# Optimization experiments

Measured on AMD Instinct MI355X. Metric: run time of the kernel, lower is better.

Reference implementation:

```python
import jax, jax.numpy as jnp
import numpy as np

N = 100000      # nodes
E = 1600000     # edges
F = 128         # num_node_features
C = 64          # graph_hidden_channels
NH = 256        # nhid
NOUT = 128      # nout
L = 4           # n_layers (hidden GCN layers)
G = 512         # number of graphs in batch


def setup_inputs() -> dict:
    key = jax.random.key(0)
    ks = jax.random.split(key, 10)
    x = jax.random.normal(ks[0], (N, F), jnp.float32)
    edge_index = jax.random.randint(ks[1], (2, E), 0, N, dtype=jnp.int64)
    batch = jnp.sort(jax.random.randint(ks[2], (N,), 0, G, dtype=jnp.int64))

    def w(k, shape, fan_in):
        return jax.random.normal(k, shape, jnp.float32) / np.float32(np.sqrt(fan_in))

    W0 = w(ks[3], (F, C), F)
    b0 = jnp.zeros((C,), jnp.float32)
    Wh = w(ks[4], (L, C, C), C)      # stacked hidden GCN weights
    bh = jnp.zeros((L, C), jnp.float32)
    W1 = w(ks[5], (C, NH), C)
    b1 = jnp.zeros((NH,), jnp.float32)
    W2 = w(ks[6], (NH, NOUT), NH)
    b2 = jnp.zeros((NOUT,), jnp.float32)
    return dict(x=x, edge_index=edge_index, batch=batch,
                W0=W0, b0=b0, Wh=Wh, bh=bh, W1=W1, b1=b1, W2=W2, b2=b2)


def _gcn_conv(h_in, W, b, src, dst, dinv):
    # PyG GCNConv: out_i = sum_{j->i} dinv_j * dinv_i * (x_j W) + dinv_i^2 * (x_i W) + b
    h = h_in @ W                                   # [N, C]
    coef = (dinv[src] * dinv[dst])[:, None]        # [E, 1]
    agg = jax.ops.segment_sum(h[src] * coef, dst, num_segments=N)
    agg = agg + h * (dinv * dinv)[:, None]         # self-loop term
    return agg + b


def reference(x, edge_index, batch, W0, b0, Wh, bh, W1, b1, W2, b2):
    src, dst = edge_index[0], edge_index[1]
    # degree with self loops (edge weight 1)
    deg = jax.ops.segment_sum(jnp.ones((E,), x.dtype), dst, num_segments=N) + 1.0
    dinv = jax.lax.rsqrt(deg)                      # [N]

    h = jax.nn.relu(_gcn_conv(x, W0, b0, src, dst, dinv))
    for i in range(L):
        h = jax.nn.relu(_gcn_conv(h, Wh[i], bh[i], src, dst, dinv))

    # global mean pool over graphs
    counts = jax.ops.segment_sum(jnp.ones((N,), x.dtype), batch, num_segments=G)
    pooled = jax.ops.segment_sum(h, batch, num_segments=G) / jnp.maximum(counts, 1.0)[:, None]

    out = jax.nn.relu(pooled @ W1 + b1)
    out = out @ W2 + b2
    return out
```

## Files before the change

kernel.cpp:

```cpp
#include <hip/hip_runtime.h>
#include <hip/hip_fp16.h>
#include <stddef.h>

static constexpr int Nn    = 100000;
static constexpr int Ee    = 1600000;
static constexpr int Ff    = 128;
static constexpr int Cc    = 64;
static constexpr int NHh   = 256;
static constexpr int NOUTt = 128;
static constexpr int Ll    = 4;
static constexpr int Gg    = 512;

static constexpr int SCAN_BLK = 1024;
static constexpr int NBLK_SCAN = (Nn + SCAN_BLK - 1) / SCAN_BLK;

static constexpr int NSUB   = (Nn + 511) / 512;
static constexpr int SUBCAP = 10240;

__global__ __launch_bounds__(256) void bin_kernel(const int* __restrict__ src,
                                                  const int* __restrict__ dst,
                                                  int* __restrict__ sb,
                                                  int* __restrict__ scnt, int E) {
    __shared__ int lcnt[NSUB], lbase[NSUB];
    const int tid = threadIdx.x;
    for (int i = tid; i < NSUB; i += 256) lcnt[i] = 0;
    __syncthreads();
    const int base = blockIdx.x * 2048;
    int pk[8], ps[8], lr[8];
    #pragma unroll
    for (int i = 0; i < 8; ++i) {
        int e = base + i * 256 + tid;
        if (e < E) {
            int d = dst[e], s = src[e];
            int sub = d >> 9;
            ps[i] = sub;
            pk[i] = s | ((d & 511) << 17);
            lr[i] = atomicAdd(&lcnt[sub], 1);
        } else ps[i] = -1;
    }
    __syncthreads();
    for (int i = tid; i < NSUB; i += 256) lbase[i] = atomicAdd(&scnt[i], lcnt[i]);
    __syncthreads();
    #pragma unroll
    for (int i = 0; i < 8; ++i) {
        if (ps[i] >= 0) {
            int pos = lbase[ps[i]] + lr[i];
            if (pos < SUBCAP) sb[(size_t)ps[i] * SUBCAP + pos] = pk[i];
        }
    }
}

__global__ __launch_bounds__(512) void cnt3_kernel(const int* __restrict__ sb,
                                                   const int* __restrict__ scnt,
                                                   int* __restrict__ cnt) {
    __shared__ int lcnt[512];
    const int sub = blockIdx.x, tid = threadIdx.x;
    lcnt[tid] = 0;
    __syncthreads();
    const int n = scnt[sub];
    const int* bp = sb + (size_t)sub * SUBCAP;
    for (int i = tid; i < n; i += 512) atomicAdd(&lcnt[(bp[i] >> 17) & 511], 1);
    __syncthreads();
    int node = sub * 512 + tid;
    if (node < Nn) cnt[node] = lcnt[tid];
}

__global__ void dinv_kernel(const int* __restrict__ cnt, float* __restrict__ dinv, int n) {
    int i = blockIdx.x * blockDim.x + threadIdx.x;
    if (i < n) dinv[i] = rsqrtf((float)cnt[i] + 1.0f);
}

__global__ __launch_bounds__(SCAN_BLK) void scan1_kernel(const int* __restrict__ cnt,
                                                         int* __restrict__ row_off,
                                                         int* __restrict__ bsum, int n) {
    __shared__ int sd[SCAN_BLK];
    int tid = threadIdx.x;
    int gid = blockIdx.x * SCAN_BLK + tid;
    int v = (gid < n) ? cnt[gid] : 0;
    sd[tid] = v;
    __syncthreads();
    #pragma unroll
    for (int off = 1; off < SCAN_BLK; off <<= 1) {
        int t = (tid >= off) ? sd[tid - off] : 0;
        __syncthreads();
        sd[tid] += t;
        __syncthreads();
    }
    if (gid < n) row_off[gid + 1] = sd[tid];
    if (tid == SCAN_BLK - 1) bsum[blockIdx.x] = sd[tid];
}

__global__ __launch_bounds__(128) void scan2_kernel(const int* __restrict__ bsum,
                                                    int* __restrict__ boff, int nb) {
    __shared__ int sd[128];
    int tid = threadIdx.x;
    sd[tid] = (tid < nb) ? bsum[tid] : 0;
    __syncthreads();
    #pragma unroll
    for (int off = 1; off < 128; off <<= 1) {
        int t = (tid >= off) ? sd[tid - off] : 0;
        __syncthreads();
        sd[tid] += t;
        __syncthreads();
    }
    if (tid < nb) boff[tid] = (tid == 0) ? 0 : sd[tid - 1];
}

__global__ void scan3_kernel(int* __restrict__ row_off, const int* __restrict__ boff, int n) {
    int gid = blockIdx.x * blockDim.x + threadIdx.x;
    if (gid < n) row_off[gid + 1] += boff[gid >> 10];
    if (gid == 0) row_off[0] = 0;
}

__global__ __launch_bounds__(512) void fill3_kernel(const int* __restrict__ sb,
                                                    const int* __restrict__ scnt,
                                                    const int* __restrict__ roff,
                                                    int* __restrict__ csr) {
    __shared__ int lcnt[512], lofs[512];
    __shared__ int gbase;
    const int sub = blockIdx.x, tid = threadIdx.x;
    lcnt[tid] = 0;
    if (tid == 0) gbase = roff[sub * 512];
    __syncthreads();
    const int n = scnt[sub];
    const int* bp = sb + (size_t)sub * SUBCAP;
    for (int i = tid; i < n; i += 512) atomicAdd(&lcnt[(bp[i] >> 17) & 511], 1);
    __syncthreads();
    int v = lcnt[tid];
    lofs[tid] = v;
    __syncthreads();
    #pragma unroll
    for (int off = 1; off < 512; off <<= 1) {
        int t = (tid >= off) ? lofs[tid - off] : 0;
        __syncthreads();
        lofs[tid] += t;
        __syncthreads();
    }
    int excl = lofs[tid] - v;
    __syncthreads();
    lcnt[tid] = excl;
    __syncthreads();
    for (int i = tid; i < n; i += 512) {
        int e = bp[i];
        int pos = atomicAdd(&lcnt[(e >> 17) & 511], 1);
        csr[gbase + pos] = e & 0x1FFFF;
    }
}

__device__ inline void add_h8(float acc[8], float4 raw) {
    const __half2* hp = reinterpret_cast<const __half2*>(&raw);
    #pragma unroll
    for (int j = 0; j < 4; ++j) {
        float2 f = __half22float2(hp[j]);
        acc[2 * j]     += f.x;
        acc[2 * j + 1] += f.y;
    }
}

__device__ inline void cvt_h8(float4 raw, float v[8]) {
    const __half2* hp = reinterpret_cast<const __half2*>(&raw);
    #pragma unroll
    for (int j = 0; j < 4; ++j) {
        float2 f = __half22float2(hp[j]);
        v[2 * j] = f.x; v[2 * j + 1] = f.y;
    }
}

__global__ __launch_bounds__(256) void gemm_xw_f32(const float* __restrict__ X,
                                                   const float* __restrict__ W,
                                                   const float* __restrict__ dinv,
                                                   __half* __restrict__ Y, int n) {
    __shared__ float hs[64][68];
    __shared__ float ws[64][64];
    const int tid = threadIdx.x;
    const int tx  = tid & 15;
    const int ty  = tid >> 4;
    const int rowbase = blockIdx.x * 64;

    float acc[4][4] = {};

    for (int k0 = 0; k0 < Ff; k0 += 64) {
        #pragma unroll
        for (int i = 0; i < 4; ++i) {
            int r = ty + i * 16;
            int gr = rowbase + r;
            float4 v = make_float4(0.f, 0.f, 0.f, 0.f);
            if (gr < n) v = *(const float4*)(X + (size_t)gr * Ff + k0 + tx * 4);
            *(float4*)&hs[r][tx * 4] = v;
        }
        #pragma unroll
        for (int i = 0; i < 4; ++i) {
            int k = ty + i * 16;
            *(float4*)&ws[k][tx * 4] = *(const float4*)(W + (size_t)(k0 + k) * 64 + tx * 4);
        }
        __syncthreads();

        #pragma unroll 4
        for (int k = 0; k < 64; ++k) {
            float4 w = *(const float4*)&ws[k][tx * 4];
            float h0 = hs[ty * 4 + 0][k];
            float h1 = hs[ty * 4 + 1][k];
            float h2 = hs[ty * 4 + 2][k];
            float h3 = hs[ty * 4 + 3][k];
            acc[0][0] += h0 * w.x; acc[0][1] += h0 * w.y; acc[0][2] += h0 * w.z; acc[0][3] += h0 * w.w;
            acc[1][0] += h1 * w.x; acc[1][1] += h1 * w.y; acc[1][2] += h1 * w.z; acc[1][3] += h1 * w.w;
            acc[2][0] += h2 * w.x; acc[2][1] += h2 * w.y; acc[2][2] += h2 * w.z; acc[2][3] += h2 * w.w;
            acc[3][0] += h3 * w.x; acc[3][1] += h3 * w.y; acc[3][2] += h3 * w.z; acc[3][3] += h3 * w.w;
        }
        __syncthreads();
    }

    #pragma unroll
    for (int i = 0; i < 4; ++i) {
        int gr = rowbase + ty * 4 + i;
        if (gr < n) {
            float di = dinv[gr];
            __half2 p0 = __floats2half2_rn(acc[i][0] * di, acc[i][1] * di);
            __half2 p1 = __floats2half2_rn(acc[i][2] * di, acc[i][3] * di);
            float2 st;
            *reinterpret_cast<__half2*>(&st.x) = p0;
            *reinterpret_cast<__half2*>(&st.y) = p1;
            *reinterpret_cast<float2*>(Y + (size_t)gr * 64 + tx * 4) = st;
        }
    }
}

__global__ __launch_bounds__(256) void gemm_xw_f16(const __half* __restrict__ X,
                                                   const float* __restrict__ W,
                                                   const float* __restrict__ dinv,
                                                   __half* __restrict__ Y, int n) {
    __shared__ float hs[64][68];
    __shared__ float ws[64][64];
    const int tid = threadIdx.x;
    const int tx  = tid & 15;
    const int ty  = tid >> 4;
    const int rowbase = blockIdx.x * 64;

    float acc[4][4] = {};

    #pragma unroll
    for (int i = 0; i < 4; ++i) {
        int r = ty + i * 16;
        int gr = rowbase + r;
        float4 v = make_float4(0.f, 0.f, 0.f, 0.f);
        if (gr < n) {
            float2 raw = *(const float2*)(X + (size_t)gr * 64 + tx * 4);
            __half2 a = *reinterpret_cast<__half2*>(&raw.x);
            __half2 b = *reinterpret_cast<__half2*>(&raw.y);
            float2 fa = __half22float2(a), fb = __half22float2(b);
            v = make_float4(fa.x, fa.y, fb.x, fb.y);
        }
        *(float4*)&hs[r][tx * 4] = v;
    }
    #pragma unroll
    for (int i = 0; i < 4; ++i) {
        int k = ty + i * 16;
        *(float4*)&ws[k][tx * 4] = *(const float4*)(W + (size_t)k * 64 + tx * 4);
    }
    __syncthreads();

    #pragma unroll 4
    for (int k = 0; k < 64; ++k) {
        float4 w = *(const float4*)&ws[k][tx * 4];
        float h0 = hs[ty * 4 + 0][k];
        float h1 = hs[ty * 4 + 1][k];
        float h2 = hs[ty * 4 + 2][k];
        float h3 = hs[ty * 4 + 3][k];
        acc[0][0] += h0 * w.x; acc[0][1] += h0 * w.y; acc[0][2] += h0 * w.z; acc[0][3] += h0 * w.w;
        acc[1][0] += h1 * w.x; acc[1][1] += h1 * w.y; acc[1][2] += h1 * w.z; acc[1][3] += h1 * w.w;
        acc[2][0] += h2 * w.x; acc[2][1] += h2 * w.y; acc[2][2] += h2 * w.z; acc[2][3] += h2 * w.w;
        acc[3][0] += h3 * w.x; acc[3][1] += h3 * w.y; acc[3][2] += h3 * w.z; acc[3][3] += h3 * w.w;
    }

    #pragma unroll
    for (int i = 0; i < 4; ++i) {
        int gr = rowbase + ty * 4 + i;
        if (gr < n) {
            float di = dinv[gr];
            __half2 p0 = __floats2half2_rn(acc[i][0] * di, acc[i][1] * di);
            __half2 p1 = __floats2half2_rn(acc[i][2] * di, acc[i][3] * di);
            float2 st;
            *reinterpret_cast<__half2*>(&st.x) = p0;
            *reinterpret_cast<__half2*>(&st.y) = p1;
            *reinterpret_cast<float2*>(Y + (size_t)gr * 64 + tx * 4) = st;
        }
    }
}

__global__ __launch_bounds__(256) void gather_agg(const int* __restrict__ row_off,
                                                  const int* __restrict__ csr_src,
                                                  const float* __restrict__ dinv,
                                                  const __half* __restrict__ t,
                                                  const float* __restrict__ b,
                                                  __half* __restrict__ out, int n) {
    const int lane = threadIdx.x & 63;
    const int node = (blockIdx.x * blockDim.x + threadIdx.x) >> 6;
    if (node >= n) return;
    const int sub = lane >> 3;
    const int c8  = lane & 7;

    const int base = row_off[node];
    const int end  = row_off[node + 1];

    float acc[8] = {};

    for (int k0 = base; k0 < end; k0 += 64) {
        int myidx = (k0 + lane < end) ? csr_src[k0 + lane] : 0;
        int nk = min(64, end - k0);
        int k = 0;
        for (; k + 16 <= nk; k += 16) {
            int s0 = __shfl(myidx, k + sub);
            int s1 = __shfl(myidx, k + 8 + sub);
            float4 r0 = *(const float4*)(t + (size_t)s0 * 64 + c8 * 8);
            float4 r1 = *(const float4*)(t + (size_t)s1 * 64 + c8 * 8);
            add_h8(acc, r0);
            add_h8(acc, r1);
        }
        for (; k < nk; k += 8) {
            int kk = k + sub;
            int s = __shfl(myidx, kk);
            if (kk < nk) {
                float4 r = *(const float4*)(t + (size_t)s * 64 + c8 * 8);
                add_h8(acc, r);
            }
        }
    }

    #pragma unroll
    for (int off = 8; off < 64; off <<= 1) {
        #pragma unroll
        for (int j = 0; j < 8; ++j) acc[j] += __shfl_xor(acc[j], off);
    }

    if (sub == 0) {
        float di = dinv[node];
        float selfv[8];
        cvt_h8(*(const float4*)(t + (size_t)node * 64 + c8 * 8), selfv);
        float4 b0 = *(const float4*)(b + c8 * 8);
        float4 b1 = *(const float4*)(b + c8 * 8 + 4);
        float bb[8] = {b0.x, b0.y, b0.z, b0.w, b1.x, b1.y, b1.z, b1.w};
        __half2 o[4];
        #pragma unroll
        for (int j = 0; j < 4; ++j) {
            float v0 = fmaxf(di * (acc[2 * j]     + selfv[2 * j])     + bb[2 * j],     0.f);
            float v1 = fmaxf(di * (acc[2 * j + 1] + selfv[2 * j + 1]) + bb[2 * j + 1], 0.f);
            o[j] = __floats2half2_rn(v0, v1);
        }
        *(float4*)(out + (size_t)node * 64 + c8 * 8) = *reinterpret_cast<float4*>(o);
    }
}

__global__ void gbounds_kernel(const int* __restrict__ batch, int* __restrict__ gstart, int n) {
    int i = blockIdx.x * blockDim.x + threadIdx.x;
    if (i >= n) return;
    int bi = batch[i];
    int bp = (i == 0) ? -1 : batch[i - 1];
    for (int g = bp + 1; g <= bi; ++g) gstart[g] = i;
    if (i == n - 1) {
        for (int g = bi + 1; g <= Gg; ++g) gstart[g] = n;
    }
}

__global__ __launch_bounds__(256) void pool_graph(const __half* __restrict__ h,
                                                  const int* __restrict__ gstart,
                                                  float* __restrict__ pooled) {
    __shared__ float sd[4][64];
    const int g    = blockIdx.x;
    const int lane = threadIdx.x & 63;
    const int wv   = threadIdx.x >> 6;
    const int s = gstart[g], e = gstart[g + 1];
    float acc = 0.f;
    for (int i = s + wv; i < e; i += 4) acc += __half2float(h[(size_t)i * 64 + lane]);
    sd[wv][lane] = acc;
    __syncthreads();
    if (wv == 0) {
        float sum = sd[0][lane] + sd[1][lane] + sd[2][lane] + sd[3][lane];
        float c = (float)(e - s);
        pooled[(size_t)g * 64 + lane] = sum / fmaxf(c, 1.f);
    }
}

__global__ void mlp1_kernel(const float* __restrict__ P, const float* __restrict__ W1,
                            const float* __restrict__ b1, float* __restrict__ H) {
    int gid = blockIdx.x * blockDim.x + threadIdx.x;
    if (gid >= Gg * NHh) return;
    int j = gid & (NHh - 1), g = gid >> 8;
    const float* p = P + (size_t)g * Cc;
    float s = b1[j];
    #pragma unroll 8
    for (int k = 0; k < Cc; ++k) s += p[k] * W1[(size_t)k * NHh + j];
    H[gid] = fmaxf(s, 0.f);
}

__global__ void mlp2_kernel(const float* __restrict__ H, const float* __restrict__ W2,
                            const float* __restrict__ b2, float* __restrict__ O) {
    int gid = blockIdx.x * blockDim.x + threadIdx.x;
    if (gid >= Gg * NOUTt) return;
    int j = gid & (NOUTt - 1), g = gid >> 7;
    const float* h = H + (size_t)g * NHh;
    float s = b2[j];
    #pragma unroll 8
    for (int k = 0; k < NHh; ++k) s += h[k] * W2[(size_t)k * NOUTt + j];
    O[gid] = s;
}

extern "C" void kernel_launch(void* const* d_in, const int* in_sizes, int n_in,
                              void* d_out, int out_size, void* d_ws, size_t ws_size,
                              hipStream_t stream) {
    const float* x     = (const float*)d_in[0];
    const int*   ei    = (const int*)  d_in[1];
    const int*   batch = (const int*)  d_in[2];
    const float* W0    = (const float*)d_in[3];
    const float* b0    = (const float*)d_in[4];
    const float* Wh    = (const float*)d_in[5];
    const float* bh    = (const float*)d_in[6];
    const float* W1    = (const float*)d_in[7];
    const float* b1    = (const float*)d_in[8];
    const float* W2    = (const float*)d_in[9];
    const float* b2    = (const float*)d_in[10];

    const int* src = ei;
    const int* dst = ei + Ee;

    char* ws = (char*)d_ws;
    constexpr size_t OFF_DINV  = 0;
    constexpr size_t OFF_CNT   = 400384;
    constexpr size_t OFF_ROFF  = OFF_CNT + 400384;
    constexpr size_t OFF_BSUM  = OFF_ROFF + 400384;
    constexpr size_t OFF_BOFF  = OFF_BSUM + 1024;
    constexpr size_t OFF_SCNT  = OFF_BOFF + 1024;
    constexpr size_t OFF_CSR   = OFF_SCNT + 1024;
    constexpr size_t OFF_T     = OFF_CSR + 6400256;
    constexpr size_t OFF_A     = OFF_T + 12800256;
    constexpr size_t OFF_POOL  = OFF_A + 12800256;
    constexpr size_t OFF_GST   = OFF_POOL + (size_t)Gg * Cc * 4;
    constexpr size_t OFF_HID   = OFF_GST + 4096;
    const size_t OFF_SB = OFF_T;

    float*  dinv   = (float*) (ws + OFF_DINV);
    int*    cnt    = (int*)   (ws + OFF_CNT);
    int*    roff   = (int*)   (ws + OFF_ROFF);
    int*    bsum   = (int*)   (ws + OFF_BSUM);
    int*    boff   = (int*)   (ws + OFF_BOFF);
    int*    scnt   = (int*)   (ws + OFF_SCNT);
    int*    csrs   = (int*)   (ws + OFF_CSR);
    int*    sb     = (int*)   (ws + OFF_SB);
    __half* T      = (__half*)(ws + OFF_T);
    __half* A      = (__half*)(ws + OFF_A);
    float*  pooled = (float*) (ws + OFF_POOL);
    int*    gstart = (int*)   (ws + OFF_GST);
    float*  hid    = (float*) (ws + OFF_HID);

    hipMemsetAsync(scnt, 0, 1024, stream);
    bin_kernel<<<(Ee + 2047) / 2048, 256, 0, stream>>>(src, dst, sb, scnt, Ee);
    cnt3_kernel<<<NSUB, 512, 0, stream>>>(sb, scnt, cnt);
    dinv_kernel<<<(Nn + 255) / 256, 256, 0, stream>>>(cnt, dinv, Nn);
    scan1_kernel<<<NBLK_SCAN, SCAN_BLK, 0, stream>>>(cnt, roff, bsum, Nn);
    scan2_kernel<<<1, 128, 0, stream>>>(bsum, boff, NBLK_SCAN);
    scan3_kernel<<<(Nn + 255) / 256, 256, 0, stream>>>(roff, boff, Nn);
    fill3_kernel<<<NSUB, 512, 0, stream>>>(sb, scnt, roff, csrs);

    gbounds_kernel<<<(Nn + 255) / 256, 256, 0, stream>>>(batch, gstart, Nn);

    const int gemm_blocks = (Nn + 63) / 64;
    const int agg_blocks  = (Nn * 64 + 255) / 256;

    gemm_xw_f32<<<gemm_blocks, 256, 0, stream>>>(x, W0, dinv, T, Nn);
    gather_agg<<<agg_blocks, 256, 0, stream>>>(roff, csrs, dinv, T, b0, A, Nn);

    for (int i = 0; i < Ll; ++i) {
        gemm_xw_f16<<<gemm_blocks, 256, 0, stream>>>(A, Wh + (size_t)i * Cc * Cc, dinv, T, Nn);
        gather_agg<<<agg_blocks, 256, 0, stream>>>(roff, csrs, dinv, T, bh + (size_t)i * Cc, A, Nn);
    }

    pool_graph<<<Gg, 256, 0, stream>>>(A, gstart, pooled);

    mlp1_kernel<<<(Gg * NHh + 255) / 256, 256, 0, stream>>>(pooled, W1, b1, hid);
    mlp2_kernel<<<(Gg * NOUTt + 255) / 256, 256, 0, stream>>>(hid, W2, b2, (float*)d_out);
}
```

Measured before the change: 406.8 us.

## Use MFMA f16 matrix cores for hidden-layer GEMMs and fuse small setup kernels

```diff
diff --git a/kernel.cpp b/kernel.cpp
--- a/kernel.cpp
+++ b/kernel.cpp
@@ -16,6 +16,9 @@
 
 static constexpr int NSUB   = (Nn + 511) / 512;
 static constexpr int SUBCAP = 10240;
+
+typedef _Float16 half8 __attribute__((ext_vector_type(8)));
+typedef float    f32x4 __attribute__((ext_vector_type(4)));
 
 __global__ __launch_bounds__(256) void bin_kernel(const int* __restrict__ src,
                                                   const int* __restrict__ dst,
@@ -52,7 +55,8 @@
 
 __global__ __launch_bounds__(512) void cnt3_kernel(const int* __restrict__ sb,
                                                    const int* __restrict__ scnt,
-                                                   int* __restrict__ cnt) {
+                                                   int* __restrict__ cnt,
+                                                   float* __restrict__ dinv) {
     __shared__ int lcnt[512];
     const int sub = blockIdx.x, tid = threadIdx.x;
     lcnt[tid] = 0;
@@ -62,12 +66,10 @@
     for (int i = tid; i < n; i += 512) atomicAdd(&lcnt[(bp[i] >> 17) & 511], 1);
     __syncthreads();
     int node = sub * 512 + tid;
-    if (node < Nn) cnt[node] = lcnt[tid];
-}
-
-__global__ void dinv_kernel(const int* __restrict__ cnt, float* __restrict__ dinv, int n) {
-    int i = blockIdx.x * blockDim.x + threadIdx.x;
-    if (i < n) dinv[i] = rsqrtf((float)cnt[i] + 1.0f);
+    if (node < Nn) {
+        cnt[node] = lcnt[tid];
+        dinv[node] = rsqrtf((float)lcnt[tid] + 1.0f);
+    }
 }
 
 __global__ __launch_bounds__(SCAN_BLK) void scan1_kernel(const int* __restrict__ cnt,
@@ -106,9 +108,18 @@
     if (tid < nb) boff[tid] = (tid == 0) ? 0 : sd[tid - 1];
 }
 
-__global__ void scan3_kernel(int* __restrict__ row_off, const int* __restrict__ boff, int n) {
+__global__ void scan3_kernel(int* __restrict__ row_off, const int* __restrict__ boff,
+                             const int* __restrict__ batch, int* __restrict__ gstart, int n) {
     int gid = blockIdx.x * blockDim.x + threadIdx.x;
-    if (gid < n) row_off[gid + 1] += boff[gid >> 10];
+    if (gid < n) {
+        row_off[gid + 1] += boff[gid >> 10];
+        int bi = batch[gid];
+        int bp = (gid == 0) ? -1 : batch[gid - 1];
+        for (int g = bp + 1; g <= bi; ++g) gstart[g] = gid;
+        if (gid == n - 1) {
+            for (int g = bi + 1; g <= Gg; ++g) gstart[g] = n;
+        }
+    }
     if (gid == 0) row_off[0] = 0;
 }
 
@@ -147,23 +158,18 @@
     }
 }
 
-__device__ inline void add_h8(float acc[8], float4 raw) {
-    const __half2* hp = reinterpret_cast<const __half2*>(&raw);
-    #pragma unroll
-    for (int j = 0; j < 4; ++j) {
-        float2 f = __half22float2(hp[j]);
-        acc[2 * j]     += f.x;
-        acc[2 * j + 1] += f.y;
-    }
-}
-
-__device__ inline void cvt_h8(float4 raw, float v[8]) {
-    const __half2* hp = reinterpret_cast<const __half2*>(&raw);
-    #pragma unroll
-    for (int j = 0; j < 4; ++j) {
-        float2 f = __half22float2(hp[j]);
-        v[2 * j] = f.x; v[2 * j + 1] = f.y;
-    }
+__global__ __launch_bounds__(512) void wcvt_kernel(const float* __restrict__ Wh,
+                                                   _Float16* __restrict__ Wf) {
+    int t = blockIdx.x * blockDim.x + threadIdx.x;
+    if (t >= 4 * 512) return;
+    int layer = t >> 9, rem = t & 511;
+    int ct = rem >> 7, c = (rem >> 6) & 1, lane = rem & 63;
+    const float* W = Wh + (size_t)layer * Cc * Cc;
+    _Float16* o = Wf + (size_t)layer * 4096 + ((size_t)(ct * 2 + c) * 64 + lane) * 8;
+    int kbase = c * 32 + (lane >> 4) * 8;
+    int col = ct * 16 + (lane & 15);
+    #pragma unroll
+    for (int j = 0; j < 8; ++j) o[j] = (_Float16)W[(kbase + j) * 64 + col];
 }
 
 __global__ __launch_bounds__(256) void gemm_xw_f32(const float* __restrict__ X,
@@ -225,65 +231,75 @@
     }
 }
 
-__global__ __launch_bounds__(256) void gemm_xw_f16(const __half* __restrict__ X,
-                                                   const float* __restrict__ W,
-                                                   const float* __restrict__ dinv,
-                                                   __half* __restrict__ Y, int n) {
-    __shared__ float hs[64][68];
-    __shared__ float ws[64][64];
-    const int tid = threadIdx.x;
-    const int tx  = tid & 15;
-    const int ty  = tid >> 4;
-    const int rowbase = blockIdx.x * 64;
-
-    float acc[4][4] = {};
-
-    #pragma unroll
-    for (int i = 0; i < 4; ++i) {
-        int r = ty + i * 16;
-        int gr = rowbase + r;
-        float4 v = make_float4(0.f, 0.f, 0.f, 0.f);
-        if (gr < n) {
-            float2 raw = *(const float2*)(X + (size_t)gr * 64 + tx * 4);
-            __half2 a = *reinterpret_cast<__half2*>(&raw.x);
-            __half2 b = *reinterpret_cast<__half2*>(&raw.y);
-            float2 fa = __half22float2(a), fb = __half22float2(b);
-            v = make_float4(fa.x, fa.y, fb.x, fb.y);
-        }
-        *(float4*)&hs[r][tx * 4] = v;
-    }
-    #pragma unroll
-    for (int i = 0; i < 4; ++i) {
-        int k = ty + i * 16;
-        *(float4*)&ws[k][tx * 4] = *(const float4*)(W + (size_t)k * 64 + tx * 4);
-    }
-    __syncthreads();
-
-    #pragma unroll 4
-    for (int k = 0; k < 64; ++k) {
-        float4 w = *(const float4*)&ws[k][tx * 4];
-        float h0 = hs[ty * 4 + 0][k];
-        float h1 = hs[ty * 4 + 1][k];
-        float h2 = hs[ty * 4 + 2][k];
-        float h3 = hs[ty * 4 + 3][k];
-        acc[0][0] += h0 * w.x; acc[0][1] += h0 * w.y; acc[0][2] += h0 * w.z; acc[0][3] += h0 * w.w;
-        acc[1][0] += h1 * w.x; acc[1][1] += h1 * w.y; acc[1][2] += h1 * w.z; acc[1][3] += h1 * w.w;
-        acc[2][0] += h2 * w.x; acc[2][1] += h2 * w.y; acc[2][2] += h2 * w.z; acc[2][3] += h2 * w.w;
-        acc[3][0] += h3 * w.x; acc[3][1] += h3 * w.y; acc[3][2] += h3 * w.z; acc[3][3] += h3 * w.w;
-    }
-
-    #pragma unroll
-    for (int i = 0; i < 4; ++i) {
-        int gr = rowbase + ty * 4 + i;
-        if (gr < n) {
-            float di = dinv[gr];
-            __half2 p0 = __floats2half2_rn(acc[i][0] * di, acc[i][1] * di);
-            __half2 p1 = __floats2half2_rn(acc[i][2] * di, acc[i][3] * di);
-            float2 st;
-            *reinterpret_cast<__half2*>(&st.x) = p0;
-            *reinterpret_cast<__half2*>(&st.y) = p1;
-            *reinterpret_cast<float2*>(Y + (size_t)gr * 64 + tx * 4) = st;
-        }
+__global__ __launch_bounds__(256) void gemm_mfma(const __half* __restrict__ A16,
+                                                 const _Float16* __restrict__ Wf,
+                                                 const float* __restrict__ dinv,
+                                                 __half* __restrict__ Y, int n) {
+    __shared__ _Float16 lds[4][1024];
+    const int tid  = threadIdx.x;
+    const int lane = tid & 63;
+    const int w    = tid >> 6;
+    const int wid  = (blockIdx.x * 256 + tid) >> 6;
+    const int ntiles = n >> 4;
+    if (wid >= ntiles) return;
+    const int node0 = wid * 16;
+
+    half8 bfrag[4][2];
+    #pragma unroll
+    for (int ct = 0; ct < 4; ++ct)
+        #pragma unroll
+        for (int c = 0; c < 2; ++c)
+            bfrag[ct][c] = *(const half8*)(Wf + ((size_t)(ct * 2 + c) * 64 + lane) * 8);
+
+    const _Float16* Ap = (const _Float16*)A16 + (size_t)(node0 + (lane & 15)) * 64 + (lane >> 4) * 8;
+    half8 afrag0 = *(const half8*)(Ap);
+    half8 afrag1 = *(const half8*)(Ap + 32);
+
+    f32x4 acc[4] = {};
+    #pragma unroll
+    for (int ct = 0; ct < 4; ++ct) {
+        acc[ct] = __builtin_amdgcn_mfma_f32_16x16x32_f16(afrag0, bfrag[ct][0], acc[ct], 0, 0, 0);
+        acc[ct] = __builtin_amdgcn_mfma_f32_16x16x32_f16(afrag1, bfrag[ct][1], acc[ct], 0, 0, 0);
+    }
+
+    const int r0 = (lane >> 4) * 4;
+    float di[4];
+    #pragma unroll
+    for (int r = 0; r < 4; ++r) di[r] = dinv[node0 + r0 + r];
+
+    #pragma unroll
+    for (int ct = 0; ct < 4; ++ct)
+        #pragma unroll
+        for (int r = 0; r < 4; ++r)
+            lds[w][(r0 + r) * 64 + ct * 16 + (lane & 15)] = (_Float16)(acc[ct][r] * di[r]);
+
+    asm volatile("s_waitcnt lgkmcnt(0)" ::: "memory");
+
+    #pragma unroll
+    for (int p = 0; p < 2; ++p) {
+        int row = p * 8 + (lane >> 3);
+        int ch  = lane & 7;
+        half8 v = *(const half8*)&lds[w][row * 64 + ch * 8];
+        *(half8*)((_Float16*)Y + (size_t)(node0 + row) * 64 + ch * 8) = v;
+    }
+}
+
+__device__ inline void add_h8(float acc[8], float4 raw) {
+    const __half2* hp = reinterpret_cast<const __half2*>(&raw);
+    #pragma unroll
+    for (int j = 0; j < 4; ++j) {
+        float2 f = __half22float2(hp[j]);
+        acc[2 * j]     += f.x;
+        acc[2 * j + 1] += f.y;
+    }
+}
+
+__device__ inline void cvt_h8(float4 raw, float v[8]) {
+    const __half2* hp = reinterpret_cast<const __half2*>(&raw);
+    #pragma unroll
+    for (int j = 0; j < 4; ++j) {
+        float2 f = __half22float2(hp[j]);
+        v[2 * j] = f.x; v[2 * j + 1] = f.y;
     }
 }
 
@@ -347,17 +363,6 @@
             o[j] = __floats2half2_rn(v0, v1);
         }
         *(float4*)(out + (size_t)node * 64 + c8 * 8) = *reinterpret_cast<float4*>(o);
-    }
-}
-
-__global__ void gbounds_kernel(const int* __restrict__ batch, int* __restrict__ gstart, int n) {
-    int i = blockIdx.x * blockDim.x + threadIdx.x;
-    if (i >= n) return;
-    int bi = batch[i];
-    int bp = (i == 0) ? -1 : batch[i - 1];
-    for (int g = bp + 1; g <= bi; ++g) gstart[g] = i;
-    if (i == n - 1) {
-        for (int g = bi + 1; g <= Gg; ++g) gstart[g] = n;
     }
 }
 
@@ -435,41 +440,42 @@
     constexpr size_t OFF_POOL  = OFF_A + 12800256;
     constexpr size_t OFF_GST   = OFF_POOL + (size_t)Gg * Cc * 4;
     constexpr size_t OFF_HID   = OFF_GST + 4096;
+    constexpr size_t OFF_WF    = OFF_HID + (size_t)Gg * NHh * 4;
     const size_t OFF_SB = OFF_T;
 
-    float*  dinv   = (float*) (ws + OFF_DINV);
-    int*    cnt    = (int*)   (ws + OFF_CNT);
-    int*    roff   = (int*)   (ws + OFF_ROFF);
-    int*    bsum   = (int*)   (ws + OFF_BSUM);
-    int*    boff   = (int*)   (ws + OFF_BOFF);
-    int*    scnt   = (int*)   (ws + OFF_SCNT);
-    int*    csrs   = (int*)   (ws + OFF_CSR);
-    int*    sb     = (int*)   (ws + OFF_SB);
-    __half* T      = (__half*)(ws + OFF_T);
-    __half* A      = (__half*)(ws + OFF_A);
-    float*  pooled = (float*) (ws + OFF_POOL);
-    int*    gstart = (int*)   (ws + OFF_GST);
-    float*  hid    = (float*) (ws + OFF_HID);
+    float*    dinv   = (float*)   (ws + OFF_DINV);
+    int*      cnt    = (int*)     (ws + OFF_CNT);
+    int*      roff   = (int*)     (ws + OFF_ROFF);
+    int*      bsum   = (int*)     (ws + OFF_BSUM);
+    int*      boff   = (int*)     (ws + OFF_BOFF);
+    int*      scnt   = (int*)     (ws + OFF_SCNT);
+    int*      csrs   = (int*)     (ws + OFF_CSR);
+    int*      sb     = (int*)     (ws + OFF_SB);
+    __half*   T      = (__half*)  (ws + OFF_T);
+    __half*   A      = (__half*)  (ws + OFF_A);
+    float*    pooled = (float*)   (ws + OFF_POOL);
+    int*      gstart = (int*)     (ws + OFF_GST);
+    float*    hid    = (float*)   (ws + OFF_HID);
+    _Float16* Wf     = (_Float16*)(ws + OFF_WF);
 
     hipMemsetAsync(scnt, 0, 1024, stream);
+    wcvt_kernel<<<4, 512, 0, stream>>>(Wh, Wf);
     bin_kernel<<<(Ee + 2047) / 2048, 256, 0, stream>>>(src, dst, sb, scnt, Ee);
-    cnt3_kernel<<<NSUB, 512, 0, stream>>>(sb, scnt, cnt);
-    dinv_kernel<<<(Nn + 255) / 256, 256, 0, stream>>>(cnt, dinv, Nn);
+    cnt3_kernel<<<NSUB, 512, 0, stream>>>(sb, scnt, cnt, dinv);
     scan1_kernel<<<NBLK_SCAN, SCAN_BLK, 0, stream>>>(cnt, roff, bsum, Nn);
     scan2_kernel<<<1, 128, 0, stream>>>(bsum, boff, NBLK_SCAN);
-    scan3_kernel<<<(Nn + 255) / 256, 256, 0, stream>>>(roff, boff, Nn);
+    scan3_kernel<<<(Nn + 255) / 256, 256, 0, stream>>>(roff, boff, batch, gstart, Nn);
     fill3_kernel<<<NSUB, 512, 0, stream>>>(sb, scnt, roff, csrs);
-
-    gbounds_kernel<<<(Nn + 255) / 256, 256, 0, stream>>>(batch, gstart, Nn);
 
     const int gemm_blocks = (Nn + 63) / 64;
     const int agg_blocks  = (Nn * 64 + 255) / 256;
+    const int mfma_blocks = ((Nn / 16) + 3) / 4;
 
     gemm_xw_f32<<<gemm_blocks, 256, 0, stream>>>(x, W0, dinv, T, Nn);
     gather_agg<<<agg_blocks, 256, 0, stream>>>(roff, csrs, dinv, T, b0, A, Nn);
 
     for (int i = 0; i < Ll; ++i) {
-        gemm_xw_f16<<<gemm_blocks, 256, 0, stream>>>(A, Wh + (size_t)i * Cc * Cc, dinv, T, Nn);
+        gemm_mfma<<<mfma_blocks, 256, 0, stream>>>(A, Wf + (size_t)i * 4096, dinv, T, Nn);
         gather_agg<<<agg_blocks, 256, 0, stream>>>(roff, csrs, dinv, T, bh + (size_t)i * Cc, A, Nn);
     }
 
```

New measurement: 372.4 us. 1.09x faster.
